# Performance work log

Hardware: AMD Instinct MI355X
Metric: run time of the kernel (lower is better)

The kernel has to match this reference:

```python
import jax, jax.numpy as jnp
import numpy as np

NUM_HEADS = 8
DIM_KEY = 64
WINDOW = 16
TEMP = float(np.power(DIM_KEY, 0.5))


def setup_inputs() -> dict:
    key = jax.random.key(0)
    k1, k2, k3, k4 = jax.random.split(key, 4)
    B, T, H = 4, 2048, 512
    std = np.sqrt(2.0 / (H + DIM_KEY))
    return {
        "query": jax.random.normal(k1, (B, T, H), dtype=jnp.float32),
        "key": jax.random.normal(k2, (B, T, H), dtype=jnp.float32),
        "Wq": jax.random.normal(k3, (NUM_HEADS * DIM_KEY, H), dtype=jnp.float32) * std,
        "bq": jnp.zeros((NUM_HEADS * DIM_KEY,), dtype=jnp.float32),
        "Wk": jax.random.normal(k4, (NUM_HEADS * DIM_KEY, H), dtype=jnp.float32) * std,
        "bk": jnp.zeros((NUM_HEADS * DIM_KEY,), dtype=jnp.float32),
    }


def reference(query, key, Wq, bq, Wk, bk):
    B, T, _ = query.shape
    w = WINDOW
    # linear projections, split into heads: [B, T, H, dk]
    q = (jnp.einsum("bti,oi->bto", query, Wq) + bq).reshape(B, T, NUM_HEADS, DIM_KEY)
    k = (jnp.einsum("bti,oi->bto", key, Wk) + bk).reshape(B, T, NUM_HEADS, DIM_KEY)
    # dense scores [B, H, Tq, Tk]
    attn = jnp.einsum("bqhd,bkhd->bhqk", q, k) / TEMP
    # window mask (get_window_mask): allowed where i-w <= j <= i+w
    i = jnp.arange(T)[:, None]
    j = jnp.arange(T)[None, :]
    allowed = (j >= i - w) & (j <= i + w)  # [T, T]
    attn = jnp.where(allowed[None, None], attn, -jnp.inf)
    attn = jax.nn.softmax(attn, axis=-1)
    # select mask gather (get_select_mask): each row keeps 2w+1 cols
    # starting at clip(i - w, 0, T - (2w+1))
    starts = jnp.clip(jnp.arange(T) - w, 0, T - (2 * w + 1))  # [T]
    idx = starts[:, None] + jnp.arange(2 * w + 1)[None, :]  # [T, 2w+1]
    out = jnp.take_along_axis(attn, idx[None, None, :, :], axis=-1)
    return out  # [B, NUM_HEADS, T, 2w+1]
```

## Files before the change

kernel.cpp:

```cpp
#include <hip/hip_runtime.h>
#include <hip/hip_bf16.h>
#include <math.h>

#define TT 2048
#define HH 512
#define NH 8
#define DK 64
#define WIN 16
#define NC 33

typedef __attribute__((ext_vector_type(8))) short bf16x8;
typedef __attribute__((ext_vector_type(4))) float f32x4;

__device__ inline ushort f2bf(float f) {
  uint u = __builtin_bit_cast(uint, f);
  return (ushort)((u + 0x7FFFu + ((u >> 16) & 1u)) >> 16);
}
__device__ inline ushort cvt1(float f) {
  __hip_bfloat16 h = __float2bfloat16(f);
  return __builtin_bit_cast(ushort, h);
}

__global__ __launch_bounds__(256) void cvt_w(
    const float* __restrict__ Wq, const float* __restrict__ Wk,
    ushort* __restrict__ Wqb, ushort* __restrict__ Wkb)
{
  const int id = blockIdx.x * 256 + threadIdx.x;
  const float* src = (id < 32768) ? Wq : Wk;
  ushort* dst = (id < 32768) ? Wqb : Wkb;
  const int off = (id & 32767) * 8;
  float4 x = *(const float4*)(src + off);
  float4 y = *(const float4*)(src + off + 4);
  union { ushort s[8]; uint4 v; } pk;
  pk.s[0]=cvt1(x.x); pk.s[1]=cvt1(x.y); pk.s[2]=cvt1(x.z); pk.s[3]=cvt1(x.w);
  pk.s[4]=cvt1(y.x); pk.s[5]=cvt1(y.y); pk.s[6]=cvt1(y.z); pk.s[7]=cvt1(y.w);
  *(uint4*)(dst + off) = pk.v;
}

#define PBM 128
#define PBN 128
#define PBK 64

__global__ __launch_bounds__(256) void proj_mfma(
    const float* __restrict__ Aq, const float* __restrict__ Ak,
    const ushort* __restrict__ Wqb, const ushort* __restrict__ Wkb,
    const float* __restrict__ bq, const float* __restrict__ bk,
    ushort* __restrict__ Qp, ushort* __restrict__ Kp)
{
  __shared__ ushort As[PBM * PBK];
  __shared__ ushort Ws[PBN * PBK];

  const int z = blockIdx.z;
  const float*  A    = z ? Ak  : Aq;
  const ushort* Wb   = z ? Wkb : Wqb;
  const float*  bias = z ? bk  : bq;
  ushort*       C    = z ? Kp  : Qp;

  const int m0 = blockIdx.x * PBM;
  const int n0 = blockIdx.y * PBN;
  const int t  = threadIdx.x;
  const int l  = t & 63;
  const int w  = t >> 6;
  const int wr = (w >> 1) * 64;
  const int wc = (w & 1) * 64;
  const int lr = l & 15;
  const int hi = l >> 4;
  const int swz = lr & 7;

  f32x4 acc[4][4] = {};

  for (int k0 = 0; k0 < HH; k0 += PBK) {
#pragma unroll
    for (int p = 0; p < 4; ++p) {
      const int u = p * 256 + t;
      const int r = u >> 3;
      const int g = (u & 7) ^ (r & 7);
      __builtin_amdgcn_global_load_lds(
          (const __attribute__((address_space(1))) uint*)
              (Wb + (size_t)(n0 + r) * HH + k0 + g * 8),
          (__attribute__((address_space(3))) uint*)(Ws + p * 2048 + w * 512),
          16, 0, 0);
    }
#pragma unroll
    for (int p = 0; p < 4; ++p) {
      const int u = p * 256 + t;
      const int r = u >> 3;
      const int g = (u & 7) ^ (r & 7);
      const float* gp = A + (size_t)(m0 + r) * HH + k0 + g * 8;
      float4 x = ((const float4*)gp)[0], y = ((const float4*)gp)[1];
      union { ushort s[8]; uint4 v; } pk;
      pk.s[0]=cvt1(x.x); pk.s[1]=cvt1(x.y); pk.s[2]=cvt1(x.z); pk.s[3]=cvt1(x.w);
      pk.s[4]=cvt1(y.x); pk.s[5]=cvt1(y.y); pk.s[6]=cvt1(y.z); pk.s[7]=cvt1(y.w);
      *(uint4*)&As[u * 8] = pk.v;
    }
    __syncthreads();

#pragma unroll
    for (int kk = 0; kk < PBK; kk += 32) {
      const int gq = (kk >> 3) + hi;
      bf16x8 af[4], bf[4];
#pragma unroll
      for (int m = 0; m < 4; ++m)
        af[m] = *(const bf16x8*)&As[(wr + m * 16 + lr) * PBK + ((gq ^ swz) * 8)];
#pragma unroll
      for (int n = 0; n < 4; ++n)
        bf[n] = *(const bf16x8*)&Ws[(wc + n * 16 + lr) * PBK + ((gq ^ swz) * 8)];
#pragma unroll
      for (int m = 0; m < 4; ++m)
#pragma unroll
        for (int n = 0; n < 4; ++n)
          acc[m][n] = __builtin_amdgcn_mfma_f32_16x16x32_bf16(af[m], bf[n], acc[m][n], 0, 0, 0);
    }
    __syncthreads();
  }

#pragma unroll
  for (int n = 0; n < 4; ++n) {
    const int col = n0 + wc + n * 16 + lr;
    const float bc = bias[col];
#pragma unroll
    for (int m = 0; m < 4; ++m) {
      const int rbase = m0 + wr + m * 16 + hi * 4;
#pragma unroll
      for (int q = 0; q < 4; ++q)
        C[(size_t)(rbase + q) * HH + col] = f2bf(acc[m][n][q] + bc);
    }
  }
}

__global__ __launch_bounds__(256) void attn_mfma(
    const ushort* __restrict__ Q, const ushort* __restrict__ Kp,
    float* __restrict__ out)
{
  const int gw = blockIdx.x * 4 + (threadIdx.x >> 6);
  const int h = gw & 7;
  const int tile = gw >> 3;
  const int b = tile >> 7;
  const int i0 = (tile & 127) * 16;
  const int l = threadIdx.x & 63;
  const int lo = l & 15;
  const int hi = l >> 4;

  int jb = i0 - WIN;
  if (jb < 0) jb = 0;
  if (jb > TT - NC) jb = TT - NC;

  const size_t qbase = ((size_t)(b * TT + i0 + lo)) * HH + h * DK + hi * 8;
  bf16x8 aq0 = *(const bf16x8*)(Q + qbase);
  bf16x8 aq1 = *(const bf16x8*)(Q + qbase + 32);

  f32x4 acc[3] = {};
#pragma unroll
  for (int a = 0; a < 3; ++a) {
    int j = jb + a * 16 + lo;
    if (j > TT - 1) j = TT - 1;
    const size_t kbase = ((size_t)(b * TT + j)) * HH + h * DK + hi * 8;
    bf16x8 bk0 = *(const bf16x8*)(Kp + kbase);
    bf16x8 bk1 = *(const bf16x8*)(Kp + kbase + 32);
    acc[a] = __builtin_amdgcn_mfma_f32_16x16x32_bf16(aq0, bk0, acc[a], 0, 0, 0);
    acc[a] = __builtin_amdgcn_mfma_f32_16x16x32_bf16(aq1, bk1, acc[a], 0, 0, 0);
  }

  float e[3][4];
  float inv[4];
#pragma unroll
  for (int q = 0; q < 4; ++q) {
    const int i = i0 + hi * 4 + q;
    const int j0 = jb + lo, j1 = j0 + 16, j2 = j0 + 32;
    float s0 = (j0 >= i - WIN && j0 <= i + WIN && j0 < TT) ? acc[0][q] * 0.125f : -INFINITY;
    float s1 = (j1 >= i - WIN && j1 <= i + WIN && j1 < TT) ? acc[1][q] * 0.125f : -INFINITY;
    float s2 = (j2 >= i - WIN && j2 <= i + WIN && j2 < TT) ? acc[2][q] * 0.125f : -INFINITY;
    float m = fmaxf(fmaxf(s0, s1), s2);
#pragma unroll
    for (int off = 8; off; off >>= 1) m = fmaxf(m, __shfl_xor(m, off));
    const float e0 = __expf(s0 - m);
    const float e1 = __expf(s1 - m);
    const float e2 = __expf(s2 - m);
    e[0][q] = e0; e[1][q] = e1; e[2][q] = e2;
    float sum = e0 + e1 + e2;
#pragma unroll
    for (int off = 8; off; off >>= 1) sum += __shfl_xor(sum, off);
    inv[q] = 1.0f / sum;
  }

  const size_t obase = ((size_t)(b * NH + h)) * TT * NC;
#pragma unroll
  for (int q = 0; q < 4; ++q) {
    const int i = i0 + hi * 4 + q;
    int st = i - WIN;
    if (st < 0) st = 0;
    if (st > TT - NC) st = TT - NC;
#pragma unroll
    for (int a = 0; a < 3; ++a) {
      const int c = jb + a * 16 + lo - st;
      if (c >= 0 && c < NC)
        out[obase + (size_t)i * NC + c] = e[a][q] * inv[q];
    }
  }
}

extern "C" void kernel_launch(void* const* d_in, const int* in_sizes, int n_in,
                              void* d_out, int out_size, void* d_ws, size_t ws_size,
                              hipStream_t stream)
{
  const float* query = (const float*)d_in[0];
  const float* key   = (const float*)d_in[1];
  const float* Wq    = (const float*)d_in[2];
  const float* bq    = (const float*)d_in[3];
  const float* Wk    = (const float*)d_in[4];
  const float* bk    = (const float*)d_in[5];
  float* out = (float*)d_out;

  const int B = 4, M = B * TT;
  ushort* Wqb = (ushort*)d_ws;
  ushort* Wkb = Wqb + (size_t)HH * HH;
  ushort* Qp  = Wkb + (size_t)HH * HH;
  ushort* Kp  = Qp + (size_t)M * HH;

  cvt_w<<<dim3(256), 256, 0, stream>>>(Wq, Wk, Wqb, Wkb);
  proj_mfma<<<dim3(M / PBM, HH / PBN, 2), 256, 0, stream>>>(
      query, key, Wqb, Wkb, bq, bk, Qp, Kp);
  attn_mfma<<<dim3((M / 16) * NH / 4), 256, 0, stream>>>(Qp, Kp, out);
}
```

Measured before the change: 35.57 us.

## Double-buffer projection GEMM LDS tiles to overlap global loads with MFMA

The projection GEMM now keeps two LDS buffers for the A and W tiles. The next k-tile's global loads, both the direct-to-LDS copy for W and the register prefetch for A, are issued before the MFMAs on the current tile. The A tile is converted to bf16 and stored after the compute. This hides global memory latency behind the matrix math and removes one barrier per iteration. In exchange it doubles LDS use to 64KB per block and adds registers for the prefetched A data, which may reduce occupancy.

```diff
diff --git a/kernel.cpp b/kernel.cpp
--- a/kernel.cpp
+++ b/kernel.cpp
@@ -40,6 +40,7 @@
 #define PBM 128
 #define PBN 128
 #define PBK 64
+#define NKI 8
 
 __global__ __launch_bounds__(256) void proj_mfma(
     const float* __restrict__ Aq, const float* __restrict__ Ak,
@@ -47,8 +48,8 @@
     const float* __restrict__ bq, const float* __restrict__ bk,
     ushort* __restrict__ Qp, ushort* __restrict__ Kp)
 {
-  __shared__ ushort As[PBM * PBK];
-  __shared__ ushort Ws[PBN * PBK];
+  __shared__ ushort As[2][PBM * PBK];
+  __shared__ ushort Ws[2][PBN * PBK];
 
   const int z = blockIdx.z;
   const float*  A    = z ? Ak  : Aq;
@@ -67,33 +68,62 @@
   const int hi = l >> 4;
   const int swz = lr & 7;
 
+  int rW[4], gW[4];
+#pragma unroll
+  for (int p = 0; p < 4; ++p) {
+    const int u = p * 256 + t;
+    rW[p] = u >> 3;
+    gW[p] = (u & 7) ^ (rW[p] & 7);
+  }
+
   f32x4 acc[4][4] = {};
 
-  for (int k0 = 0; k0 < HH; k0 += PBK) {
+#pragma unroll
+  for (int p = 0; p < 4; ++p)
+    __builtin_amdgcn_global_load_lds(
+        (const __attribute__((address_space(1))) uint*)
+            (Wb + (size_t)(n0 + rW[p]) * HH + gW[p] * 8),
+        (__attribute__((address_space(3))) uint*)(&Ws[0][p * 2048 + w * 512]),
+        16, 0, 0);
+  {
+    float4 ax[4], ay[4];
 #pragma unroll
     for (int p = 0; p < 4; ++p) {
-      const int u = p * 256 + t;
-      const int r = u >> 3;
-      const int g = (u & 7) ^ (r & 7);
-      __builtin_amdgcn_global_load_lds(
-          (const __attribute__((address_space(1))) uint*)
-              (Wb + (size_t)(n0 + r) * HH + k0 + g * 8),
-          (__attribute__((address_space(3))) uint*)(Ws + p * 2048 + w * 512),
-          16, 0, 0);
+      const float* gp = A + (size_t)(m0 + rW[p]) * HH + gW[p] * 8;
+      ax[p] = ((const float4*)gp)[0];
+      ay[p] = ((const float4*)gp)[1];
     }
 #pragma unroll
     for (int p = 0; p < 4; ++p) {
-      const int u = p * 256 + t;
-      const int r = u >> 3;
-      const int g = (u & 7) ^ (r & 7);
-      const float* gp = A + (size_t)(m0 + r) * HH + k0 + g * 8;
-      float4 x = ((const float4*)gp)[0], y = ((const float4*)gp)[1];
       union { ushort s[8]; uint4 v; } pk;
-      pk.s[0]=cvt1(x.x); pk.s[1]=cvt1(x.y); pk.s[2]=cvt1(x.z); pk.s[3]=cvt1(x.w);
-      pk.s[4]=cvt1(y.x); pk.s[5]=cvt1(y.y); pk.s[6]=cvt1(y.z); pk.s[7]=cvt1(y.w);
-      *(uint4*)&As[u * 8] = pk.v;
-    }
-    __syncthreads();
+      pk.s[0]=cvt1(ax[p].x); pk.s[1]=cvt1(ax[p].y); pk.s[2]=cvt1(ax[p].z); pk.s[3]=cvt1(ax[p].w);
+      pk.s[4]=cvt1(ay[p].x); pk.s[5]=cvt1(ay[p].y); pk.s[6]=cvt1(ay[p].z); pk.s[7]=cvt1(ay[p].w);
+      *(uint4*)&As[0][(p * 256 + t) * 8] = pk.v;
+    }
+  }
+  __syncthreads();
+
+#pragma unroll
+  for (int tt = 0; tt < NKI; ++tt) {
+    const int cur = tt & 1, nxt = cur ^ 1;
+    const int k1 = (tt + 1) * PBK;
+
+    float4 ax[4], ay[4];
+    if (tt < NKI - 1) {
+#pragma unroll
+      for (int p = 0; p < 4; ++p)
+        __builtin_amdgcn_global_load_lds(
+            (const __attribute__((address_space(1))) uint*)
+                (Wb + (size_t)(n0 + rW[p]) * HH + k1 + gW[p] * 8),
+            (__attribute__((address_space(3))) uint*)(&Ws[nxt][p * 2048 + w * 512]),
+            16, 0, 0);
+#pragma unroll
+      for (int p = 0; p < 4; ++p) {
+        const float* gp = A + (size_t)(m0 + rW[p]) * HH + k1 + gW[p] * 8;
+        ax[p] = ((const float4*)gp)[0];
+        ay[p] = ((const float4*)gp)[1];
+      }
+    }
 
 #pragma unroll
     for (int kk = 0; kk < PBK; kk += 32) {
@@ -101,15 +131,25 @@
       bf16x8 af[4], bf[4];
 #pragma unroll
       for (int m = 0; m < 4; ++m)
-        af[m] = *(const bf16x8*)&As[(wr + m * 16 + lr) * PBK + ((gq ^ swz) * 8)];
+        af[m] = *(const bf16x8*)&As[cur][(wr + m * 16 + lr) * PBK + ((gq ^ swz) * 8)];
 #pragma unroll
       for (int n = 0; n < 4; ++n)
-        bf[n] = *(const bf16x8*)&Ws[(wc + n * 16 + lr) * PBK + ((gq ^ swz) * 8)];
+        bf[n] = *(const bf16x8*)&Ws[cur][(wc + n * 16 + lr) * PBK + ((gq ^ swz) * 8)];
 #pragma unroll
       for (int m = 0; m < 4; ++m)
 #pragma unroll
         for (int n = 0; n < 4; ++n)
           acc[m][n] = __builtin_amdgcn_mfma_f32_16x16x32_bf16(af[m], bf[n], acc[m][n], 0, 0, 0);
+    }
+
+    if (tt < NKI - 1) {
+#pragma unroll
+      for (int p = 0; p < 4; ++p) {
+        union { ushort s[8]; uint4 v; } pk;
+        pk.s[0]=cvt1(ax[p].x); pk.s[1]=cvt1(ax[p].y); pk.s[2]=cvt1(ax[p].z); pk.s[3]=cvt1(ax[p].w);
+        pk.s[4]=cvt1(ay[p].x); pk.s[5]=cvt1(ay[p].y); pk.s[6]=cvt1(ay[p].z); pk.s[7]=cvt1(ay[p].w);
+        *(uint4*)&As[nxt][(p * 256 + t) * 8] = pk.v;
+      }
     }
     __syncthreads();
   }
```

Measured after the change: 35.64 us. Within noise of the previous version (+0.2%).
